# Optimization experiments

Hardware: AMD Instinct MI355X
Metric: run time of the kernel (lower is better)

The kernel has to match this reference:

```python
import jax, jax.numpy as jnp
import numpy as np
import math

B, S, D, K = 8, 2048, 1024, 64
EPS = 1e-5

def _ln(x):
    m = jnp.mean(x, axis=-1, keepdims=True)
    v = jnp.mean((x - m) ** 2, axis=-1, keepdims=True)
    return (x - m) * jax.lax.rsqrt(v + EPS)

def setup_inputs() -> dict:
    key = jax.random.key(0)
    ks = jax.random.split(key, 14)
    s = 0.02
    return {
        "x":  jax.random.normal(ks[0], (B, S, D), dtype=jnp.float32),
        "Wk": jax.random.normal(ks[1], (D, K), dtype=jnp.float32) * s,
        "bk": jnp.zeros((K,), dtype=jnp.float32),
        "Wq": jax.random.normal(ks[2], (D, K), dtype=jnp.float32) * s,
        "bq": jnp.zeros((K,), dtype=jnp.float32),
        "Wv": jax.random.normal(ks[3], (D, D), dtype=jnp.float32) * s,
        "bv": jnp.zeros((D,), dtype=jnp.float32),
        "Wb": jax.random.normal(ks[4], (D, 1), dtype=jnp.float32) * s,
        "bb": jnp.zeros((1,), dtype=jnp.float32),
        "W1": jax.random.normal(ks[5], (D, D), dtype=jnp.float32) * s,
        "b1": jnp.zeros((D,), dtype=jnp.float32),
        "g1": jnp.ones((D,), dtype=jnp.float32),
        "be1": jnp.zeros((D,), dtype=jnp.float32),
    }

def reference(x, Wk, bk, Wq, bq, Wv, bv, Wb, bb, W1, b1, g1, be1):
    scale = 1.0 / math.sqrt(K)
    keys    = (jnp.einsum('bsd,dk->bsk', x, Wk) + bk) * scale   # [B,S,K]
    queries = jnp.einsum('bsd,dk->bsk', x, Wq) + bq             # [B,S,K]
    values  = jnp.einsum('bsd,de->bse', x, Wv) + bv             # [B,S,D]
    biases  = jnp.einsum('bsd,do->bso', x, Wb) + bb             # [B,S,1]
    # scores[b,i,j] = keys[b,i] . queries[b,j] + biases[b,i]
    scores = jax.nn.sigmoid(jnp.einsum('bik,bjk->bij', keys, queries) + biases)
    attention = jnp.einsum('bij,bjd->bid', scores, values)      # [B,S,D]
    res = _ln(x + attention) * g1 + be1
    feedforward = jax.nn.relu(jnp.einsum('bsd,de->bse', res, W1) + b1)
    return _ln(res + feedforward)
```

## Files before the change

### kernel.cpp

```cpp
#include <hip/hip_runtime.h>
#include <math.h>


typedef __bf16 bf16_t;
typedef __bf16 bf16x4_t __attribute__((ext_vector_type(4)));
typedef __bf16 bf16x8_t __attribute__((ext_vector_type(8)));
typedef float  f32x4    __attribute__((ext_vector_type(4)));

#define DEV static __device__ __forceinline__

DEV void gll16(const void* g, void* l) {
  __builtin_amdgcn_global_load_lds(
      (const __attribute__((address_space(1))) void*)g,
      (__attribute__((address_space(3))) void*)l, 16, 0, 0);
}

template <int MODE, int MFAST>
__global__ __launch_bounds__(512, 2) void gemm256(
    const bf16_t* __restrict__ A, const bf16_t* __restrict__ B,
    bf16_t* __restrict__ C, int K, int lda, int ldb, int ldc,
    long sAb, long sBb, long sCb, const float* __restrict__ aux0) {
  const int gx = gridDim.x, gy = gridDim.y;
  const int gxy = gx * gy;
  const int nwg = gxy * (int)gridDim.z;
  const int orig = blockIdx.x + gx * blockIdx.y + gxy * blockIdx.z;
  const int lid = (orig & 7) * (nwg >> 3) + (orig >> 3);
  const int bz = lid / gxy;
  const int rem = lid - bz * gxy;
  const int bx = MFAST ? (rem / gy) : (rem % gx);
  const int by = MFAST ? (rem % gy) : (rem / gx);

  A += (long)bz * sAb;
  B += (long)bz * sBb;
  const int m0 = by * 256, n0 = bx * 256;

  __shared__ bf16_t SM[65536];
#define ASH(b, h) (&SM[(((b)*2 + (h)) << 13)])
#define BSH(b, h) (&SM[32768 + (((b)*2 + (h)) << 13)])

  const int tid = threadIdx.x;
  const int wid = tid >> 6, l = tid & 63;
  const int wr = wid >> 2, wc = wid & 3;
  const int lr = l & 15, lh = l >> 4;

  const int sRow = tid >> 2;
  const int sSl = (tid & 3) ^ ((tid >> 3) & 3);
  const bf16_t* Asrc = A + (long)(m0 + sRow) * lda + sSl * 8;
  const bf16_t* Bsrc = B + (long)(n0 + sRow) * ldb + sSl * 8;
  const long aStep = (long)128 * lda, bStep = (long)128 * ldb;

#define STAGE_A(b, h, kt) do { \
    const bf16_t* s_ = Asrc + (kt) * 64 + (h) * 32; \
    gll16(s_,         ASH(b, h) + tid * 8); \
    gll16(s_ + aStep, ASH(b, h) + 4096 + tid * 8); } while (0)
#define STAGE_B(b, h, kt) do { \
    const bf16_t* s_ = Bsrc + (kt) * 64 + (h) * 32; \
    gll16(s_,         BSH(b, h) + tid * 8); \
    gll16(s_ + bStep, BSH(b, h) + 4096 + tid * 8); } while (0)

  const int sw = (lh ^ ((lr >> 1) & 3)) * 8;
  const int aOff = (wr * 128 + lr) * 32 + sw;
  const int bOff = (wc * 64 + lr) * 32 + sw;

  f32x4 acc[8][4] = {};
  const int NT = K >> 6;

  STAGE_A(0, 0, 0); STAGE_B(0, 0, 0); STAGE_A(0, 1, 0); STAGE_B(0, 1, 0);
  asm volatile("s_waitcnt vmcnt(4)" ::: "memory");
  __builtin_amdgcn_s_barrier();

#define PHASE_SYNC() do { \
    __builtin_amdgcn_sched_barrier(0); \
    __builtin_amdgcn_s_barrier(); \
    asm volatile("s_waitcnt lgkmcnt(0)" ::: "memory"); \
    __builtin_amdgcn_sched_barrier(0); } while (0)
#define MFMA_LO() do { \
    __builtin_amdgcn_s_setprio(1); \
    _Pragma("unroll") for (int m = 0; m < 4; ++m) \
    _Pragma("unroll") for (int n = 0; n < 4; ++n) \
      acc[m][n] = __builtin_amdgcn_mfma_f32_16x16x32_bf16(aF[m], bF[n], acc[m][n], 0, 0, 0); \
    __builtin_amdgcn_s_setprio(0); } while (0)
#define MFMA_HI() do { \
    __builtin_amdgcn_s_setprio(1); \
    _Pragma("unroll") for (int m = 0; m < 4; ++m) \
    _Pragma("unroll") for (int n = 0; n < 4; ++n) \
      acc[m + 4][n] = __builtin_amdgcn_mfma_f32_16x16x32_bf16(aG[m], bF[n], acc[m + 4][n], 0, 0, 0); \
    __builtin_amdgcn_s_setprio(0); } while (0)

  for (int t = 0; t < NT; ++t) {
    const int p = t & 1, q = p ^ 1;
    const bool pf = (t + 1 < NT);
    bf16x8_t bF[4], aF[4], aG[4];

#pragma unroll
    for (int n = 0; n < 4; ++n) bF[n] = *(const bf16x8_t*)(BSH(p, 0) + bOff + n * 512);
#pragma unroll
    for (int m = 0; m < 4; ++m) aF[m] = *(const bf16x8_t*)(ASH(p, 0) + aOff + m * 512);
    if (pf) STAGE_A(q, 0, t + 1);
    PHASE_SYNC();
    MFMA_LO();

#pragma unroll
    for (int m = 0; m < 4; ++m) aG[m] = *(const bf16x8_t*)(ASH(p, 0) + aOff + (m + 4) * 512);
    if (pf) {
      STAGE_B(q, 0, t + 1);
      asm volatile("s_waitcnt vmcnt(4)" ::: "memory");
    } else {
      asm volatile("s_waitcnt vmcnt(0)" ::: "memory");
    }
    PHASE_SYNC();
    MFMA_HI();

#pragma unroll
    for (int n = 0; n < 4; ++n) bF[n] = *(const bf16x8_t*)(BSH(p, 1) + bOff + n * 512);
#pragma unroll
    for (int m = 0; m < 4; ++m) aF[m] = *(const bf16x8_t*)(ASH(p, 1) + aOff + m * 512);
    if (pf) STAGE_A(q, 1, t + 1);
    PHASE_SYNC();
    MFMA_LO();

#pragma unroll
    for (int m = 0; m < 4; ++m) aG[m] = *(const bf16x8_t*)(ASH(p, 1) + aOff + (m + 4) * 512);
    if (pf) STAGE_B(q, 1, t + 1);
    asm volatile("s_waitcnt vmcnt(4)" ::: "memory");
    PHASE_SYNC();
    MFMA_HI();
  }
#undef STAGE_A
#undef STAGE_B
#undef PHASE_SYNC
#undef MFMA_LO
#undef MFMA_HI

  __builtin_amdgcn_s_barrier();
  {
    const int rowb = wr * 128 + lh * 4;
    const int colb = wc * 64 + lr;
#pragma unroll
    for (int m = 0; m < 8; ++m)
#pragma unroll
      for (int n = 0; n < 4; ++n) {
        const f32x4 v = acc[m][n];
        const int cl = colb + n * 16;
#pragma unroll
        for (int r = 0; r < 4; ++r) {
          const int rl = rowb + m * 16 + r;
          float val = v[r];
          if constexpr (MODE == 1) val += aux0[m0 + rl];
          else if constexpr (MODE == 4) val = fmaxf(val + aux0[n0 + cl], 0.0f);
          SM[rl * 256 + (cl ^ (lh << 4))] = (bf16_t)val;
        }
      }
    __builtin_amdgcn_s_barrier();
    bf16_t* Cb = C + (long)bz * sCb;
    const int chunk = tid & 31, rsub = tid >> 5;
#pragma unroll
    for (int pp = 0; pp < 16; ++pp) {
      const int rl = pp * 16 + rsub;
      const int sc = chunk ^ (((rl >> 2) & 3) << 1);
      const bf16x8_t vv = *(const bf16x8_t*)&SM[rl * 256 + sc * 8];
      *(bf16x8_t*)&Cb[(long)(m0 + rl) * ldc + n0 + chunk * 8] = vv;
    }
  }
#undef ASH
#undef BSH
}

template <int MODE, int MFAST>
__global__ __launch_bounds__(256) void gemm_bt(
    const bf16_t* __restrict__ A, const bf16_t* __restrict__ B,
    void* __restrict__ Cv, int M, int N, int K, int lda, int ldb, int ldc,
    long sAb, long sBb, long sCb,
    const float* __restrict__ aux0, const float* __restrict__ aux1, long sAux) {
  const int gx = gridDim.x, gy = gridDim.y;
  const int gxy = gx * gy;
  const int nwg = gxy * (int)gridDim.z;
  const int orig = blockIdx.x + gx * blockIdx.y + gxy * blockIdx.z;
  const int q = nwg >> 3, r8 = nwg & 7;
  const int xcd = orig & 7, seq = orig >> 3;
  const int lid = (xcd < r8 ? xcd * (q + 1) : r8 * (q + 1) + (xcd - r8) * q) + seq;
  const int bz = lid / gxy;
  const int rem = lid - bz * gxy;
  const int bx = MFAST ? (rem / gy) : (rem % gx);
  const int by = MFAST ? (rem % gy) : (rem / gx);

  A += (long)bz * sAb;
  B += (long)bz * sBb;
  const float* a0 = (MODE == 2) ? (aux0 + (long)bz * sAux) : aux0;

  const int m0 = by * 128;
  const int n0 = bx * 128;

  __shared__ bf16_t SM[16384];
#define ASH(b) (&SM[(b) << 12])
#define BSH(b) (&SM[8192 + ((b) << 12)])

  const int tid = threadIdx.x;
  const int w = tid >> 6, l = tid & 63;
  const int wr = w >> 1, wc = w & 1;
  const int lr = l & 15, lh = l >> 4;

  const int srow = l >> 2;
  const int scol = (((l & 3) ^ (srow & 3)) << 3);

  f32x4 acc[4][4] = {};

  auto stage = [&](int buf, int k0) {
#pragma unroll
    for (int half = 0; half < 2; ++half) {
      const int i = 2 * w + half;
      const int row = (i << 4) + srow;
      gll16(A + (long)(m0 + row) * lda + k0 + scol, ASH(buf) + (i << 9));
      gll16(B + (long)(n0 + row) * ldb + k0 + scol, BSH(buf) + (i << 9));
    }
  };

  stage(0, 0);
  __syncthreads();
  int cur = 0;
  const int sw = ((lh ^ (lr & 3)) << 3);

  for (int k0 = 0; k0 < K; k0 += 32) {
    if (k0 + 32 < K) stage(cur ^ 1, k0 + 32);

    bf16x8_t af[4], bfm[4];
#pragma unroll
    for (int m = 0; m < 4; ++m)
      af[m] = *(const bf16x8_t*)(ASH(cur) + (((wr << 6) + (m << 4) + lr) << 5) + sw);
#pragma unroll
    for (int n = 0; n < 4; ++n)
      bfm[n] = *(const bf16x8_t*)(BSH(cur) + (((wc << 6) + (n << 4) + lr) << 5) + sw);
#pragma unroll
    for (int m = 0; m < 4; ++m)
#pragma unroll
      for (int n = 0; n < 4; ++n)
        acc[m][n] = __builtin_amdgcn_mfma_f32_16x16x32_bf16(af[m], bfm[n], acc[m][n], 0, 0, 0);

    __syncthreads();
    cur ^= 1;
  }

  {
    const int rowb = (wr << 6) + (lh << 2);
    const int colb = (wc << 6) + lr;
#pragma unroll
    for (int m = 0; m < 4; ++m)
#pragma unroll
      for (int n = 0; n < 4; ++n) {
        const f32x4 v = acc[m][n];
        const int cl = colb + (n << 4);
#pragma unroll
        for (int r = 0; r < 4; ++r) {
          const int rl = rowb + (m << 4) + r;
          float val = v[r];
          if constexpr (MODE == 0) {
            const int cc = n0 + cl;
            const float b = (cc < 64) ? aux0[cc] : aux1[cc - 64];
            val = (cc < 64) ? (val + b) * 0.125f : (val + b);
          } else {
            const float zz = val + a0[m0 + rl];
            val = __builtin_amdgcn_rcpf(1.0f + __expf(-zz));
          }
          SM[rl * 128 + (cl ^ (lh << 4))] = (bf16_t)val;
        }
      }
    __syncthreads();
    bf16_t* Cb = (bf16_t*)Cv + (MODE == 2 ? (long)bz * sCb : 0L);
    const int chunk = tid & 15, rsub = tid >> 4;
#pragma unroll
    for (int pp = 0; pp < 8; ++pp) {
      const int rl = pp * 16 + rsub;
      const int sc = chunk ^ (((rl >> 2) & 3) << 1);
      const bf16x8_t vv = *(const bf16x8_t*)&SM[rl * 128 + sc * 8];
      *(bf16x8_t*)&Cb[(long)(m0 + rl) * ldc + n0 + chunk * 8] = vv;
    }
  }
#undef ASH
#undef BSH
}

__global__ __launch_bounds__(256) void cast_bias_kernel(
    const float* __restrict__ x, const float* __restrict__ Wb,
    const float* __restrict__ bb, bf16_t* __restrict__ x_bf,
    float* __restrict__ biases) {
  const int r = blockIdx.x * 4 + (threadIdx.x >> 6);
  const int l = threadIdx.x & 63;
  const float* xr = x + (long)r * 1024;
  bf16_t* orow = x_bf + (long)r * 1024;
  float s = 0.f;
#pragma unroll
  for (int i = 0; i < 4; ++i) {
    const int off = l * 4 + i * 256;
    const float4 v = *(const float4*)(xr + off);
    const float4 w = *(const float4*)(Wb + off);
    s += v.x * w.x + v.y * w.y + v.z * w.z + v.w * w.w;
    bf16x4_t o;
    o[0] = (bf16_t)v.x; o[1] = (bf16_t)v.y; o[2] = (bf16_t)v.z; o[3] = (bf16_t)v.w;
    *(bf16x4_t*)(orow + off) = o;
  }
#pragma unroll
  for (int off = 1; off < 64; off <<= 1) s += __shfl_xor(s, off);
  if (l == 0) biases[r] = s + bb[0];
}

__global__ __launch_bounds__(256) void transpose_cast_kernel(
    const float* __restrict__ in, bf16_t* __restrict__ out, int R, int C) {
  __shared__ float t[32][33];
  const int c0 = blockIdx.x * 32, r0 = blockIdx.y * 32;
  const int tx = threadIdx.x & 31, ty = threadIdx.x >> 5;
#pragma unroll
  for (int i = 0; i < 4; ++i) {
    const int rl = ty * 4 + i;
    t[rl][tx] = in[(long)(r0 + rl) * C + c0 + tx];
  }
  __syncthreads();
#pragma unroll
  for (int i = 0; i < 4; ++i) {
    const int rl = ty * 4 + i;
    out[(long)(c0 + rl) * R + r0 + tx] = (bf16_t)t[tx][rl];
  }
}

DEV float2 block_sum2(float s, float ss) {
#pragma unroll
  for (int off = 1; off < 64; off <<= 1) {
    s += __shfl_xor(s, off);
    ss += __shfl_xor(ss, off);
  }
  __shared__ float bs[4], bss[4];
  const int w = threadIdx.x >> 6, l = threadIdx.x & 63;
  if (l == 0) { bs[w] = s; bss[w] = ss; }
  __syncthreads();
  s = bs[0] + bs[1] + bs[2] + bs[3];
  ss = bss[0] + bss[1] + bss[2] + bss[3];
  return make_float2(s, ss);
}

__global__ __launch_bounds__(256) void ln1_kernel(
    const bf16_t* __restrict__ x, const bf16_t* __restrict__ attn,
    const float* __restrict__ g, const float* __restrict__ be,
    bf16_t* __restrict__ res) {
  const long r = blockIdx.x;
  const int t = threadIdx.x;
  const bf16x4_t xv = *(const bf16x4_t*)(x + r * 1024 + t * 4);
  const bf16x4_t av = *(const bf16x4_t*)(attn + r * 1024 + t * 4);
  const float y0 = (float)xv[0] + (float)av[0], y1 = (float)xv[1] + (float)av[1];
  const float y2 = (float)xv[2] + (float)av[2], y3 = (float)xv[3] + (float)av[3];
  const float2 s2 = block_sum2(y0 + y1 + y2 + y3, y0 * y0 + y1 * y1 + y2 * y2 + y3 * y3);
  const float mean = s2.x * (1.0f / 1024.0f);
  const float var = s2.y * (1.0f / 1024.0f) - mean * mean;
  const float rs = rsqrtf(var + 1e-5f);
  const int c = t * 4;
  bf16x4_t o;
  o[0] = (bf16_t)((y0 - mean) * rs * g[c + 0] + be[c + 0]);
  o[1] = (bf16_t)((y1 - mean) * rs * g[c + 1] + be[c + 1]);
  o[2] = (bf16_t)((y2 - mean) * rs * g[c + 2] + be[c + 2]);
  o[3] = (bf16_t)((y3 - mean) * rs * g[c + 3] + be[c + 3]);
  *(bf16x4_t*)(res + r * 1024 + c) = o;
}

__global__ __launch_bounds__(256) void ln2_kernel(
    const bf16_t* __restrict__ res, const bf16_t* __restrict__ h,
    float* __restrict__ out) {
  const long r = blockIdx.x;
  const int t = threadIdx.x;
  const bf16x4_t rv = *(const bf16x4_t*)(res + r * 1024 + t * 4);
  const bf16x4_t hv = *(const bf16x4_t*)(h + r * 1024 + t * 4);
  const float y0 = (float)rv[0] + (float)hv[0], y1 = (float)rv[1] + (float)hv[1];
  const float y2 = (float)rv[2] + (float)hv[2], y3 = (float)rv[3] + (float)hv[3];
  const float2 s2 = block_sum2(y0 + y1 + y2 + y3, y0 * y0 + y1 * y1 + y2 * y2 + y3 * y3);
  const float mean = s2.x * (1.0f / 1024.0f);
  const float var = s2.y * (1.0f / 1024.0f) - mean * mean;
  const float rs = rsqrtf(var + 1e-5f);
  float4 o;
  o.x = (y0 - mean) * rs; o.y = (y1 - mean) * rs;
  o.z = (y2 - mean) * rs; o.w = (y3 - mean) * rs;
  ((float4*)(out + r * 1024))[t] = o;
}

extern "C" void kernel_launch(void* const* d_in, const int* in_sizes, int n_in,
                              void* d_out, int out_size, void* d_ws, size_t ws_size,
                              hipStream_t stream) {
  const float* x   = (const float*)d_in[0];
  const float* Wk  = (const float*)d_in[1];
  const float* bk  = (const float*)d_in[2];
  const float* Wq  = (const float*)d_in[3];
  const float* bq  = (const float*)d_in[4];
  const float* Wv  = (const float*)d_in[5];
  const float* bv  = (const float*)d_in[6];
  const float* Wb  = (const float*)d_in[7];
  const float* bb  = (const float*)d_in[8];
  const float* W1  = (const float*)d_in[9];
  const float* b1  = (const float*)d_in[10];
  const float* g1  = (const float*)d_in[11];
  const float* be1 = (const float*)d_in[12];
  float* out = (float*)d_out;

  char* ws = (char*)d_ws;
  bf16_t* x_bf    = (bf16_t*)(ws + 0);
  bf16_t* vt_bf   = (bf16_t*)(ws + 33554432);
  bf16_t* kq_bf   = (bf16_t*)(ws + 67108864);
  bf16_t* Wkqt    = (bf16_t*)(ws + 71303168);
  bf16_t* Wvt     = (bf16_t*)(ws + 71565312);
  bf16_t* W1t     = (bf16_t*)(ws + 73662464);
  float*  biases  = (float*) (ws + 75759616);
  bf16_t* scores  = (bf16_t*)(ws + 75825152);
  bf16_t* attn_bf = (bf16_t*)(ws + 142934016);
  bf16_t* res_bf  = (bf16_t*)(ws + 176488448);
  bf16_t* h_bf    = attn_bf;

  cast_bias_kernel<<<4096, 256, 0, stream>>>(x, Wb, bb, x_bf, biases);
  transpose_cast_kernel<<<dim3(2, 32), 256, 0, stream>>>(Wk, Wkqt, 1024, 64);
  transpose_cast_kernel<<<dim3(2, 32), 256, 0, stream>>>(Wq, Wkqt + 64 * 1024, 1024, 64);
  transpose_cast_kernel<<<dim3(32, 32), 256, 0, stream>>>(Wv, Wvt, 1024, 1024);
  transpose_cast_kernel<<<dim3(32, 32), 256, 0, stream>>>(W1, W1t, 1024, 1024);

  gemm_bt<0, 0><<<dim3(1, 128, 1), 256, 0, stream>>>(
      x_bf, Wkqt, kq_bf, 16384, 128, 1024, 1024, 1024, 128, 0, 0, 0, bk, bq, 0);

  gemm256<1, 1><<<dim3(64, 4, 1), 512, 0, stream>>>(
      Wvt, x_bf, vt_bf, 1024, 1024, 1024, 16384, 0, 0, 0, bv);

  gemm_bt<2, 0><<<dim3(16, 16, 8), 256, 0, stream>>>(
      kq_bf, kq_bf + 64, scores, 2048, 2048, 64, 128, 128, 2048,
      2048L * 128, 2048L * 128, 2048L * 2048, biases, nullptr, 2048);

  gemm256<3, 0><<<dim3(4, 8, 8), 512, 0, stream>>>(
      scores, vt_bf, attn_bf, 2048, 2048, 16384, 1024,
      2048L * 2048, 2048, 2048L * 1024, nullptr);

  ln1_kernel<<<16384, 256, 0, stream>>>(x_bf, attn_bf, g1, be1, res_bf);

  gemm256<4, 0><<<dim3(4, 64, 1), 512, 0, stream>>>(
      res_bf, W1t, h_bf, 1024, 1024, 1024, 1024, 0, 0, 0, b1);

  ln2_kernel<<<16384, 256, 0, stream>>>(res_bf, h_bf, out);
}
```

Before: 252.4 us.

## Add thin KQ projection kernel and store gemm256 epilogue directly to global

```diff
diff --git a/kernel.cpp b/kernel.cpp
--- a/kernel.cpp
+++ b/kernel.cpp
@@ -132,34 +132,104 @@
 #undef MFMA_LO
 #undef MFMA_HI
 
-  __builtin_amdgcn_s_barrier();
-  {
-    const int rowb = wr * 128 + lh * 4;
-    const int colb = wc * 64 + lr;
-#pragma unroll
-    for (int m = 0; m < 8; ++m)
-#pragma unroll
-      for (int n = 0; n < 4; ++n) {
-        const f32x4 v = acc[m][n];
-        const int cl = colb + n * 16;
-#pragma unroll
-        for (int r = 0; r < 4; ++r) {
-          const int rl = rowb + m * 16 + r;
-          float val = v[r];
-          if constexpr (MODE == 1) val += aux0[m0 + rl];
-          else if constexpr (MODE == 4) val = fmaxf(val + aux0[n0 + cl], 0.0f);
-          SM[rl * 256 + (cl ^ (lh << 4))] = (bf16_t)val;
+  bf16_t* Cb = C + (long)bz * sCb;
+  const int rowb = m0 + wr * 128 + lh * 4;
+  const int colb = n0 + wc * 64 + lr;
+#pragma unroll
+  for (int m = 0; m < 8; ++m)
+#pragma unroll
+    for (int n = 0; n < 4; ++n) {
+      const f32x4 v = acc[m][n];
+      const int cc = colb + n * 16;
+#pragma unroll
+      for (int r = 0; r < 4; ++r) {
+        const int rr = rowb + m * 16 + r;
+        const float val = v[r];
+        if constexpr (MODE == 1) {
+          Cb[(long)rr * ldc + cc] = (bf16_t)(val + aux0[rr]);
+        } else if constexpr (MODE == 3) {
+          Cb[(long)rr * ldc + cc] = (bf16_t)val;
+        } else {
+          Cb[(long)rr * ldc + cc] = (bf16_t)fmaxf(val + aux0[cc], 0.0f);
         }
       }
-    __builtin_amdgcn_s_barrier();
-    bf16_t* Cb = C + (long)bz * sCb;
-    const int chunk = tid & 31, rsub = tid >> 5;
-#pragma unroll
-    for (int pp = 0; pp < 16; ++pp) {
+    }
+#undef ASH
+#undef BSH
+}
+
+__global__ __launch_bounds__(256) void kq_thin(
+    const bf16_t* __restrict__ A, const bf16_t* __restrict__ B,
+    bf16_t* __restrict__ C,
+    const float* __restrict__ bk, const float* __restrict__ bq) {
+  const int m0 = blockIdx.x * 64;
+
+  __shared__ bf16_t SM[12288];
+#define ASH(b) (&SM[(b) << 11])
+#define BSH(b) (&SM[4096 + ((b) << 12)])
+
+  const int tid = threadIdx.x;
+  const int w = tid >> 6, l = tid & 63;
+  const int lr = l & 15, lh = l >> 4;
+
+  const int sRow = tid >> 2;
+  const int sSl = (tid & 3) ^ ((tid >> 3) & 3);
+  const bf16_t* Asrc = A + (long)(m0 + sRow) * 1024 + sSl * 8;
+  const bf16_t* Bsrc0 = B + (long)sRow * 1024 + sSl * 8;
+  const bf16_t* Bsrc1 = B + (long)(64 + sRow) * 1024 + sSl * 8;
+
+  const int sw = (lh ^ ((lr >> 1) & 3)) * 8;
+  const int aOff = (w * 16 + lr) * 32 + sw;
+
+  f32x4 acc[8] = {};
+
+  auto stage = [&](int buf, int k0) {
+    gll16(Asrc + k0, ASH(buf) + tid * 8);
+    gll16(Bsrc0 + k0, BSH(buf) + tid * 8);
+    gll16(Bsrc1 + k0, BSH(buf) + 2048 + tid * 8);
+  };
+
+  stage(0, 0);
+  __syncthreads();
+  int cur = 0;
+
+  for (int k0 = 0; k0 < 1024; k0 += 32) {
+    if (k0 + 32 < 1024) stage(cur ^ 1, k0 + 32);
+
+    const bf16x8_t aF = *(const bf16x8_t*)(ASH(cur) + aOff);
+    bf16x8_t bF[8];
+#pragma unroll
+    for (int j = 0; j < 8; ++j)
+      bF[j] = *(const bf16x8_t*)(BSH(cur) + (j * 16 + lr) * 32 + sw);
+#pragma unroll
+    for (int j = 0; j < 8; ++j)
+      acc[j] = __builtin_amdgcn_mfma_f32_16x16x32_bf16(aF, bF[j], acc[j], 0, 0, 0);
+
+    __syncthreads();
+    cur ^= 1;
+  }
+
+  {
+#pragma unroll
+    for (int j = 0; j < 8; ++j) {
+      const f32x4 v = acc[j];
+      const int cl = j * 16 + lr;
+      const float b = (cl < 64) ? bk[cl] : bq[cl - 64];
+      const float s = (cl < 64) ? 0.125f : 1.0f;
+#pragma unroll
+      for (int r = 0; r < 4; ++r) {
+        const int rl = w * 16 + lh * 4 + r;
+        SM[rl * 128 + (cl ^ (lh << 4))] = (bf16_t)((v[r] + b) * s);
+      }
+    }
+    __syncthreads();
+    const int chunk = tid & 15, rsub = tid >> 4;
+#pragma unroll
+    for (int pp = 0; pp < 4; ++pp) {
       const int rl = pp * 16 + rsub;
       const int sc = chunk ^ (((rl >> 2) & 3) << 1);
-      const bf16x8_t vv = *(const bf16x8_t*)&SM[rl * 256 + sc * 8];
-      *(bf16x8_t*)&Cb[(long)(m0 + rl) * ldc + n0 + chunk * 8] = vv;
+      const bf16x8_t vv = *(const bf16x8_t*)&SM[rl * 128 + sc * 8];
+      *(bf16x8_t*)&C[(long)(m0 + rl) * 128 + chunk * 8] = vv;
     }
   }
 #undef ASH
@@ -252,20 +322,13 @@
 #pragma unroll
         for (int r = 0; r < 4; ++r) {
           const int rl = rowb + (m << 4) + r;
-          float val = v[r];
-          if constexpr (MODE == 0) {
-            const int cc = n0 + cl;
-            const float b = (cc < 64) ? aux0[cc] : aux1[cc - 64];
-            val = (cc < 64) ? (val + b) * 0.125f : (val + b);
-          } else {
-            const float zz = val + a0[m0 + rl];
-            val = __builtin_amdgcn_rcpf(1.0f + __expf(-zz));
-          }
-          SM[rl * 128 + (cl ^ (lh << 4))] = (bf16_t)val;
+          const float zz = v[r] + a0[m0 + rl];
+          SM[rl * 128 + (cl ^ (lh << 4))] =
+              (bf16_t)__builtin_amdgcn_rcpf(1.0f + __expf(-zz));
         }
       }
     __syncthreads();
-    bf16_t* Cb = (bf16_t*)Cv + (MODE == 2 ? (long)bz * sCb : 0L);
+    bf16_t* Cb = (bf16_t*)Cv + (long)bz * sCb;
     const int chunk = tid & 15, rsub = tid >> 4;
 #pragma unroll
     for (int pp = 0; pp < 8; ++pp) {
@@ -415,8 +478,7 @@
   transpose_cast_kernel<<<dim3(32, 32), 256, 0, stream>>>(Wv, Wvt, 1024, 1024);
   transpose_cast_kernel<<<dim3(32, 32), 256, 0, stream>>>(W1, W1t, 1024, 1024);
 
-  gemm_bt<0, 0><<<dim3(1, 128, 1), 256, 0, stream>>>(
-      x_bf, Wkqt, kq_bf, 16384, 128, 1024, 1024, 1024, 128, 0, 0, 0, bk, bq, 0);
+  kq_thin<<<256, 256, 0, stream>>>(x_bf, Wkqt, kq_bf, bk, bq);
 
   gemm256<1, 1><<<dim3(64, 4, 1), 512, 0, stream>>>(
       Wvt, x_bf, vt_bf, 1024, 1024, 1024, 16384, 0, 0, 0, bv);
```

New measurement: 241.6 us. -4.3%, faster.
